# Performance work log

Hardware: AMD Instinct MI355X
Metric: run time of the kernel (lower is better)

Reference implementation:

```python
import jax, jax.numpy as jnp
import numpy as np

N, T, E = 50000, 12, 800000
IN_C, HID, OUT_C = 32, 64, 32


def setup_inputs() -> dict:
    key = jax.random.key(0)
    ks = jax.random.split(key, 20)
    def lin(k, fan_in, shape):
        b = 1.0 / np.sqrt(fan_in)
        return jax.random.uniform(k, shape, jnp.float32, -b, b)
    inp = {
        "x": jax.random.normal(ks[0], (T, N, IN_C), jnp.float32),
        "edge_index": jax.random.randint(ks[1], (T, 2, E), 0, N, jnp.int32),
        "edge_weight": jax.random.uniform(ks[2], (T, E), jnp.float32),
        # GCNConv weights (x @ W, glorot) + biases for z, r, h gates
        "Wz": lin(ks[3], IN_C, (IN_C, HID)), "bz": jnp.zeros((HID,), jnp.float32),
        "Wr": lin(ks[4], IN_C, (IN_C, HID)), "br": jnp.zeros((HID,), jnp.float32),
        "Wh": lin(ks[5], IN_C, (IN_C, HID)), "bh": jnp.zeros((HID,), jnp.float32),
        # Linear(2*hidden -> hidden) for each gate
        "Lz_w": lin(ks[6], 2 * HID, (2 * HID, HID)), "Lz_b": lin(ks[7], 2 * HID, (HID,)),
        "Lr_w": lin(ks[8], 2 * HID, (2 * HID, HID)), "Lr_b": lin(ks[9], 2 * HID, (HID,)),
        "Lh_w": lin(ks[10], 2 * HID, (2 * HID, HID)), "Lh_b": lin(ks[11], 2 * HID, (HID,)),
        # final Linear(hidden -> out)
        "W_out": lin(ks[12], HID, (HID, OUT_C)), "b_out": lin(ks[13], HID, (OUT_C,)),
    }
    return inp


def _gcn_conv(x, src, dst, ew, W, b):
    # GCNConv with add_self_loops=True, symmetric gcn_norm
    loop = jnp.arange(N, dtype=src.dtype)
    s = jnp.concatenate([src, loop])
    d = jnp.concatenate([dst, loop])
    w = jnp.concatenate([ew, jnp.ones((N,), ew.dtype)])
    deg = jax.ops.segment_sum(w, d, num_segments=N)          # [N]
    dinv = jnp.where(deg > 0, jax.lax.rsqrt(deg), 0.0)
    norm = dinv[s] * w * dinv[d]                              # [E+N]
    h = x @ W                                                 # [N, HID]
    out = jax.ops.segment_sum(h[s] * norm[:, None], d, num_segments=N)
    return out + b


def _tgcn_step(x, src, dst, ew, p):
    # H is zeros every call (model never threads hidden state)
    H = jnp.zeros((N, HID), x.dtype)
    cz = _gcn_conv(x, src, dst, ew, p["Wz"], p["bz"])
    Z = jax.nn.sigmoid(jnp.concatenate([cz, H], axis=1) @ p["Lz_w"] + p["Lz_b"])
    cr = _gcn_conv(x, src, dst, ew, p["Wr"], p["br"])
    R = jax.nn.sigmoid(jnp.concatenate([cr, H], axis=1) @ p["Lr_w"] + p["Lr_b"])
    ch = _gcn_conv(x, src, dst, ew, p["Wh"], p["bh"])
    Ht = jnp.tanh(jnp.concatenate([ch, H * R], axis=1) @ p["Lh_w"] + p["Lh_b"])
    return Z * H + (1.0 - Z) * Ht


def reference(x, edge_index, edge_weight, Wz, bz, Wr, br, Wh, bh,
              Lz_w, Lz_b, Lr_w, Lr_b, Lh_w, Lh_b, W_out, b_out):
    p = dict(Wz=Wz, bz=bz, Wr=Wr, br=br, Wh=Wh, bh=bh,
             Lz_w=Lz_w, Lz_b=Lz_b, Lr_w=Lr_w, Lr_b=Lr_b, Lh_w=Lh_w, Lh_b=Lh_b)

    def step(acc, ts):
        xt, ei, ew = ts
        out = _tgcn_step(xt, ei[0], ei[1], ew, p)
        return acc + out, None

    acc, _ = jax.lax.scan(step, jnp.zeros((N, HID), x.dtype),
                          (x, edge_index, edge_weight))
    mean = acc / T
    return mean @ W_out + b_out
```

## Files before the change

### kernel.cpp

```cpp
#include <hip/hip_runtime.h>
#include <hip/hip_fp16.h>

#define NN 50000
#define TT 12
#define EE 800000
#define IN_C 32
#define HID 64
#define OUT_C 32
#define BSZ 64
#define NB ((NN + BSZ - 1) / BSZ)
#define EPB 8192
#define ABLK ((EE + EPB - 1) / EPB)
#define BST 512
#define GT 4
#define XPAIRS ((size_t)TT * NN * 16)

typedef _Float16 half8_t __attribute__((ext_vector_type(8)));
typedef float f32x4_t __attribute__((ext_vector_type(4)));

__global__ __launch_bounds__(64) void prep_kernel(
    const float* __restrict__ Wz, const float* __restrict__ bz,
    const float* __restrict__ Lzw, const float* __restrict__ Lzb,
    const float* __restrict__ Wh, const float* __restrict__ bh,
    const float* __restrict__ Lhw, const float* __restrict__ Lhb,
    float* __restrict__ Mz, float* __restrict__ Bz,
    float* __restrict__ Mh, float* __restrict__ Bh) {
  const int j = threadIdx.x;
  const int i = blockIdx.x;
  const int h = blockIdx.y;
  const float* W  = h ? Wh  : Wz;
  const float* b  = h ? bh  : bz;
  const float* L  = h ? Lhw : Lzw;
  const float* Lb = h ? Lhb : Lzb;
  float* M = h ? Mh : Mz;
  float* B = h ? Bh : Bz;
  if (i < IN_C) {
    float v = 0.f;
    for (int k = 0; k < HID; ++k) v += W[i * HID + k] * L[k * HID + j];
    M[i * HID + j] = v;
  } else {
    float v = Lb[j];
    for (int k = 0; k < HID; ++k) v += b[k] * L[k * HID + j];
    B[j] = v;
  }
}

__global__ __launch_bounds__(64) void prep_b16_kernel(
    const float* __restrict__ Mz, const float* __restrict__ Mh,
    _Float16* __restrict__ B16) {
  int l = threadIdx.x;
  int cc = blockIdx.x;
  int g = blockIdx.y;
  const float* M = g ? Mh : Mz;
#pragma unroll
  for (int i = 0; i < 8; ++i) {
    int k = (l >> 4) * 8 + i;
    int col = cc * 16 + (l & 15);
    B16[(((size_t)g * 4 + cc) * 64 + l) * 8 + i] = (_Float16)M[k * HID + col];
  }
}

__global__ __launch_bounds__(256) void xconv_kernel(const float* __restrict__ x,
                                                    __half2* __restrict__ xh) {
  size_t i = (size_t)blockIdx.x * 256 + threadIdx.x;
  if (i < XPAIRS) {
    float2 f = ((const float2*)x)[i];
    xh[i] = __floats2half2_rn(f.x, f.y);
  }
}

__global__ __launch_bounds__(BST) void bsort_kernel(
    const int* __restrict__ ei, const float* __restrict__ ew,
    unsigned long long* __restrict__ bin2G, int* __restrict__ runoffG,
    int tbase) {
  __shared__ int hist[NB];
  __shared__ int rnk[NB];
  __shared__ int lbase[NB + 1];
  __shared__ unsigned long long sent[EPB];
  int tl = blockIdx.y;
  const int* src = ei + (size_t)(tbase + tl) * 2 * EE;
  const int* dst = src + EE;
  const float* w = ew + (size_t)(tbase + tl) * EE;
  int t = threadIdx.x;
  for (int i = t; i < NB; i += BST) { hist[i] = 0; rnk[i] = 0; }
  __syncthreads();
  int e0 = blockIdx.x * EPB;
  int cnt = min(EPB, EE - e0);
  for (int i = t; i < cnt; i += BST) atomicAdd(&hist[dst[e0 + i] >> 6], 1);
  __syncthreads();
  if (t == 0) {
    int run = 0;
    for (int b = 0; b < NB; ++b) { lbase[b] = run; run += hist[b]; }
    lbase[NB] = run;
  }
  __syncthreads();
  int* rof = runoffG + ((size_t)tl * ABLK + blockIdx.x) * (NB + 1);
  for (int b = t; b < NB + 1; b += BST) rof[b] = lbase[b];
  for (int i = t; i < cnt; i += BST) {
    int d = dst[e0 + i], s = src[e0 + i];
    int b = d >> 6;
    unsigned short hw = __half_as_ushort(__float2half_rn(w[e0 + i]));
    int pos = lbase[b] + atomicAdd(&rnk[b], 1);
    sent[pos] = (unsigned long long)((unsigned)s | ((unsigned)(d & 63) << 16)) |
                ((unsigned long long)hw << 32);
  }
  __syncthreads();
  unsigned long long* reg = bin2G + ((size_t)tl * ABLK + blockIdx.x) * EPB;
  for (int i = t; i < cnt; i += BST) reg[i] = sent[i];
}

__global__ __launch_bounds__(256) void deg_kernel(
    const int* __restrict__ runoffG, const unsigned long long* __restrict__ bin2G,
    float* __restrict__ dinvA, int* __restrict__ loffA) {
  __shared__ float wsum[BSZ];
  __shared__ int cnt[BSZ];
  __shared__ int loff[BSZ];
  int tl = blockIdx.y, b = blockIdx.x;
  int t = threadIdx.x;
  if (t < BSZ) { wsum[t] = 0.f; cnt[t] = 0; }
  __syncthreads();
  const int* runoff = runoffG + (size_t)tl * ABLK * (NB + 1);
  int g = t >> 5;
  int lane = t & 31;
  for (int blk = g; blk < ABLK; blk += 8) {
    int r0 = runoff[blk * (NB + 1) + b];
    int r1 = runoff[blk * (NB + 1) + b + 1];
    const unsigned long long* reg = bin2G + ((size_t)tl * ABLK + blk) * EPB;
    for (int i = r0 + lane; i < r1; i += 32) {
      unsigned long long u = reg[i];
      int dl = (int)((u >> 16) & 63u);
      atomicAdd(&wsum[dl], __half2float(__ushort_as_half((unsigned short)(u >> 32))));
      atomicAdd(&cnt[dl], 1);
    }
  }
  __syncthreads();
  if (t == 0) {
    int run = 0;
#pragma unroll
    for (int i = 0; i < BSZ; ++i) { loff[i] = run; run += cnt[i]; }
  }
  __syncthreads();
  int n = b * BSZ + t;
  if (t < BSZ && n < NN) {
    dinvA[(size_t)tl * NN + n] = rsqrtf(1.0f + wsum[t]);
    loffA[(size_t)tl * NN + n] = loff[t];
  }
}

__global__ __launch_bounds__(1024) void bscan_kernel(const int* __restrict__ runoffG,
                                                     int* __restrict__ bbaseA) {
  __shared__ int s[1024];
  int tl = blockIdx.x, t = threadIdx.x;
  const int* runoff = runoffG + (size_t)tl * ABLK * (NB + 1);
  int v = 0;
  if (t < NB) {
    for (int blk = 0; blk < ABLK; ++blk)
      v += runoff[blk * (NB + 1) + t + 1] - runoff[blk * (NB + 1) + t];
  }
  s[t] = v;
  __syncthreads();
  for (int o = 1; o < 1024; o <<= 1) {
    int u = (t >= o) ? s[t - o] : 0;
    __syncthreads();
    s[t] += u;
    __syncthreads();
  }
  if (t < NB) bbaseA[(size_t)tl * NB + t] = s[t] - v;
}

__global__ __launch_bounds__(256) void sort_kernel(
    const int* __restrict__ runoffG, const unsigned long long* __restrict__ bin2G,
    const float* __restrict__ dinvA, const int* __restrict__ bbaseA,
    const int* __restrict__ loffA, unsigned* __restrict__ sbufG,
    int* __restrict__ noffG) {
  __shared__ int plc[BSZ];
  int tl = blockIdx.y, b = blockIdx.x;
  int t = threadIdx.x;
  int base = bbaseA[(size_t)tl * NB + b];
  int* noff = noffG + (size_t)tl * (NN + 1);
  if (t < BSZ) {
    int n = b * BSZ + t;
    int v = (n < NN) ? base + loffA[(size_t)tl * NN + n] : base;
    plc[t] = v;
    if (n < NN) noff[n] = v;
  }
  if (b == 0 && t == 0) noff[NN] = EE;
  __syncthreads();
  const int* runoff = runoffG + (size_t)tl * ABLK * (NB + 1);
  const float* dinv = dinvA + (size_t)tl * NN;
  unsigned* sbuf = sbufG + (size_t)tl * EE;
  int g = t >> 5;
  int lane = t & 31;
  for (int blk = g; blk < ABLK; blk += 8) {
    int r0 = runoff[blk * (NB + 1) + b];
    int r1 = runoff[blk * (NB + 1) + b + 1];
    const unsigned long long* reg = bin2G + ((size_t)tl * ABLK + blk) * EPB;
    for (int i = r0 + lane; i < r1; i += 32) {
      unsigned long long u = reg[i];
      int s = (int)(u & 0xFFFFu);
      int dl = (int)((u >> 16) & 63u);
      float nm = __half2float(__ushort_as_half((unsigned short)(u >> 32))) * dinv[s];
      int pos = atomicAdd(&plc[dl], 1);
      sbuf[pos] = (unsigned)s |
                  ((unsigned)__half_as_ushort(__float2half_rn(nm)) << 16);
    }
  }
}

__global__ __launch_bounds__(256) void gather_y_kernel(
    const __half2* __restrict__ xh,
    const float* __restrict__ dinvA, const int* __restrict__ noffG,
    const unsigned* __restrict__ sbufG, __half2* __restrict__ yG, int tbase) {
  int t = threadIdx.x;
  int w = t >> 6;
  int lane = t & 63;
  int h2 = lane >> 5;
  int g = (lane >> 2) & 7;
  int cq = lane & 3;
  int tl = blockIdx.y;
  int n = blockIdx.x * 8 + w * 2 + h2;

  const float* dinv = dinvA + (size_t)tl * NN;
  const int* noff = noffG + (size_t)tl * (NN + 1);
  const unsigned* sbuf = sbufG + (size_t)tl * EE;
  const __half2* xht = xh + (size_t)(tbase + tl) * NN * 16;

  int e0 = noff[n], e1 = noff[n + 1];
  float v0 = 0.f, v1 = 0.f, v2 = 0.f, v3 = 0.f;
  float v4 = 0.f, v5 = 0.f, v6 = 0.f, v7 = 0.f;
  for (int e = e0 + g; e < e1; e += 8) {
    unsigned u = sbuf[e];
    float nm = __half2float(__ushort_as_half((unsigned short)(u >> 16)));
    uint4 xr = ((const uint4*)(xht + (size_t)(u & 0xFFFFu) * 16))[cq];
    const __half2* hp = (const __half2*)&xr;
    float2 f0 = __half22float2(hp[0]);
    float2 f1 = __half22float2(hp[1]);
    float2 f2 = __half22float2(hp[2]);
    float2 f3 = __half22float2(hp[3]);
    v0 += nm * f0.x; v1 += nm * f0.y;
    v2 += nm * f1.x; v3 += nm * f1.y;
    v4 += nm * f2.x; v5 += nm * f2.y;
    v6 += nm * f3.x; v7 += nm * f3.y;
  }
#pragma unroll
  for (int m = 4; m <= 16; m <<= 1) {
    v0 += __shfl_xor(v0, m); v1 += __shfl_xor(v1, m);
    v2 += __shfl_xor(v2, m); v3 += __shfl_xor(v3, m);
    v4 += __shfl_xor(v4, m); v5 += __shfl_xor(v5, m);
    v6 += __shfl_xor(v6, m); v7 += __shfl_xor(v7, m);
  }
  if (g == 0) {
    float dv = dinv[n];
    uint4 xs = ((const uint4*)(xht + (size_t)n * 16))[cq];
    const __half2* hs = (const __half2*)&xs;
    float2 s0 = __half22float2(hs[0]);
    float2 s1 = __half22float2(hs[1]);
    float2 s2 = __half22float2(hs[2]);
    float2 s3 = __half22float2(hs[3]);
    __half2 o[4];
    o[0] = __floats2half2_rn(dv * (v0 + dv * s0.x), dv * (v1 + dv * s0.y));
    o[1] = __floats2half2_rn(dv * (v2 + dv * s1.x), dv * (v3 + dv * s1.y));
    o[2] = __floats2half2_rn(dv * (v4 + dv * s2.x), dv * (v5 + dv * s2.y));
    o[3] = __floats2half2_rn(dv * (v6 + dv * s3.x), dv * (v7 + dv * s3.y));
    __half2* yp = yG + ((size_t)tl * NN + n) * 16 + cq * 4;
    *(uint4*)yp = *(const uint4*)o;
  }
}

__global__ __launch_bounds__(256) void gate_acc_kernel(
    const __half2* __restrict__ yG, const _Float16* __restrict__ B16,
    const float* __restrict__ Bz, const float* __restrict__ Bh,
    float* __restrict__ acc, int c) {
  int t = threadIdx.x;
  int w = t >> 6;
  int lane = t & 63;
  int nb = blockIdx.x * BSZ;
  int t0 = blockIdx.y * GT;
  int te = min(t0 + GT, c);

  half8_t bf[8];
#pragma unroll
  for (int q = 0; q < 8; ++q)
    bf[q] = *(const half8_t*)(B16 + ((size_t)q * 64 + lane) * 8);
  float bzv[4], bhv[4];
#pragma unroll
  for (int cc = 0; cc < 4; ++cc) {
    bzv[cc] = Bz[cc * 16 + (lane & 15)];
    bhv[cc] = Bh[cc * 16 + (lane & 15)];
  }
  float accr[16];
#pragma unroll
  for (int k = 0; k < 16; ++k) accr[k] = 0.f;

  const _Float16* yF = (const _Float16*)yG;
  int arow = nb + w * 16 + (lane & 15);
  if (arow >= NN) arow = NN - 1;
  int koff = (lane >> 4) * 8;

  for (int tl = t0; tl < te; ++tl) {
    half8_t a = *(const half8_t*)(yF + ((size_t)tl * NN + arow) * 32 + koff);
    f32x4_t dz0 = {0.f, 0.f, 0.f, 0.f};
    f32x4_t dz[4], dh[4];
#pragma unroll
    for (int cc = 0; cc < 4; ++cc) {
      dz[cc] = __builtin_amdgcn_mfma_f32_16x16x32_f16(a, bf[cc], dz0, 0, 0, 0);
      dh[cc] = __builtin_amdgcn_mfma_f32_16x16x32_f16(a, bf[4 + cc], dz0, 0, 0, 0);
    }
#pragma unroll
    for (int cc = 0; cc < 4; ++cc) {
#pragma unroll
      for (int r = 0; r < 4; ++r) {
        float za = dz[cc][r] + bzv[cc];
        float ha = dh[cc][r] + bhv[cc];
        float z = 1.0f / (1.0f + __expf(-za));
        float th = 1.0f - 2.0f / (__expf(2.f * ha) + 1.0f);
        accr[cc * 4 + r] += (1.0f - z) * th;
      }
    }
  }
#pragma unroll
  for (int cc = 0; cc < 4; ++cc) {
#pragma unroll
    for (int r = 0; r < 4; ++r) {
      int n = nb + w * 16 + (lane >> 4) * 4 + r;
      int j = cc * 16 + (lane & 15);
      if (n < NN) atomicAdd(&acc[(size_t)n * HID + j], accr[cc * 4 + r]);
    }
  }
}

__global__ __launch_bounds__(256) void out_kernel(const float* __restrict__ acc,
                                                  const float* __restrict__ W_out,
                                                  const float* __restrict__ b_out,
                                                  float* __restrict__ out) {
  __shared__ float sW[HID * OUT_C], sB[OUT_C];
  for (int i = threadIdx.x; i < HID * OUT_C; i += 256) sW[i] = W_out[i];
  if (threadIdx.x < OUT_C) sB[threadIdx.x] = b_out[threadIdx.x];
  __syncthreads();
  unsigned tid = blockIdx.x * 256u + threadIdx.x;
  unsigned n = tid >> 5;
  int o = tid & 31;
  if (n >= NN) return;
  const float* ar = acc + (size_t)n * HID;
  float v = 0.f;
#pragma unroll
  for (int k = 0; k < HID; ++k) v += ar[k] * sW[k * OUT_C + o];
  out[(size_t)n * OUT_C + o] = v * (1.0f / (float)TT) + sB[o];
}

static inline char* alignp(char* p, size_t a) {
  return (char*)(((size_t)p + a - 1) & ~(a - 1));
}

extern "C" void kernel_launch(void* const* d_in, const int* in_sizes, int n_in,
                              void* d_out, int out_size, void* d_ws, size_t ws_size,
                              hipStream_t stream) {
  const float* x     = (const float*)d_in[0];
  const int*   ei    = (const int*)d_in[1];
  const float* ew    = (const float*)d_in[2];
  const float* Wz    = (const float*)d_in[3];
  const float* bz    = (const float*)d_in[4];
  const float* Wh    = (const float*)d_in[7];
  const float* bh    = (const float*)d_in[8];
  const float* Lz_w  = (const float*)d_in[9];
  const float* Lz_b  = (const float*)d_in[10];
  const float* Lh_w  = (const float*)d_in[13];
  const float* Lh_b  = (const float*)d_in[14];
  const float* W_out = (const float*)d_in[15];
  const float* b_out = (const float*)d_in[16];
  float* out = (float*)d_out;

  const size_t noffB  = (size_t)(NN + 1) * 4;
  const size_t dinvB  = (size_t)NN * 4;
  const size_t loffB  = (size_t)NN * 4;
  const size_t bbB    = (size_t)NB * 4;
  const size_t rofB   = (size_t)ABLK * (NB + 1) * 4;
  const size_t sbufB  = (size_t)EE * 4;
  const size_t bin2B  = (size_t)ABLK * EPB * 8;
  const size_t perT   = noffB + dinvB + loffB + bbB + rofB + sbufB + bin2B;
  const size_t xhB    = XPAIRS * 4;
  const size_t fixedB = 4 * ((size_t)2 * IN_C * HID + 2 * HID)
                      + 8192 + (size_t)NN * HID * 4 + xhB + 4096;

  int nt = 12;
  if (ws_size < fixedB + 12 * perT) {
    nt = (int)((ws_size - fixedB) / perT);
    if (nt < 1) nt = 1;
    if (nt > 12) nt = 12;
  }

  char* p = (char*)d_ws;
  unsigned long long* bin2 = (unsigned long long*)p;
  p += bin2B * nt;
  int* noffG  = (int*)p;          p += noffB * nt;
  float* dinv = (float*)p;        p += dinvB * nt;
  int* loffG  = (int*)p;          p += loffB * nt;
  int* bbase  = (int*)p;          p += bbB * nt;
  int* runoff = (int*)p;          p += rofB * nt;
  unsigned* sbufG = (unsigned*)p; p += sbufB * nt;
  p = alignp(p, 16);
  _Float16* B16 = (_Float16*)p;   p += 8192;
  float* Mz = (float*)p;
  float* Mh = Mz + IN_C * HID;
  float* Bz = Mh + IN_C * HID;
  float* Bh = Bz + HID;
  float* acc = Bh + HID;
  p = alignp((char*)(acc + (size_t)NN * HID), 256);
  __half2* xh = (__half2*)p;
  __half2* yG = (__half2*)bin2;

  prep_kernel<<<dim3(IN_C + 1, 2), 64, 0, stream>>>(Wz, bz, Lz_w, Lz_b, Wh, bh,
                                                    Lh_w, Lh_b, Mz, Bz, Mh, Bh);
  prep_b16_kernel<<<dim3(4, 2), 64, 0, stream>>>(Mz, Mh, B16);
  xconv_kernel<<<(unsigned)((XPAIRS + 255) / 256), 256, 0, stream>>>(x, xh);
  hipMemsetAsync(acc, 0, (size_t)NN * HID * sizeof(float), stream);

  for (int tb = 0; tb < TT; tb += nt) {
    int c = (TT - tb < nt) ? (TT - tb) : nt;
    bsort_kernel<<<dim3(ABLK, c), BST, 0, stream>>>(ei, ew, bin2, runoff, tb);
    deg_kernel<<<dim3(NB, c), 256, 0, stream>>>(runoff, bin2, dinv, loffG);
    bscan_kernel<<<c, 1024, 0, stream>>>(runoff, bbase);
    sort_kernel<<<dim3(NB, c), 256, 0, stream>>>(runoff, bin2, dinv, bbase,
                                                 loffG, sbufG, noffG);
    gather_y_kernel<<<dim3(NN / 8, c), 256, 0, stream>>>(xh, dinv, noffG,
                                                         sbufG, yG, tb);
    gate_acc_kernel<<<dim3(NB, (c + GT - 1) / GT), 256, 0, stream>>>(
        yG, B16, Bz, Bh, acc, c);
  }

  out_kernel<<<(NN * OUT_C + 255) / 256, 256, 0, stream>>>(acc, W_out, b_out, out);
}
```

Before: 533.4 us.

## Fuse degree and sort kernels, defer source-dinv scaling to gather

Merges deg_kernel and sort_kernel into one sortdeg_kernel that computes per-node weight sums and local offsets in shared memory, then scatters edges in the same block. The loffA buffer and one launch go away, and the binned edge list is read twice inside one block instead of across two kernels. Because dinv[src] is not yet known during sorting, the source-side dinv multiply moves into gather_y_kernel, which adds a random dinv load per edge there. The sort now stores the raw half edge weight.

```diff
diff --git a/kernel.cpp b/kernel.cpp
--- a/kernel.cpp
+++ b/kernel.cpp
@@ -109,11 +109,34 @@
   for (int i = t; i < cnt; i += BST) reg[i] = sent[i];
 }
 
-__global__ __launch_bounds__(256) void deg_kernel(
+__global__ __launch_bounds__(1024) void bscan_kernel(const int* __restrict__ runoffG,
+                                                     int* __restrict__ bbaseA) {
+  __shared__ int s[1024];
+  int tl = blockIdx.x, t = threadIdx.x;
+  const int* runoff = runoffG + (size_t)tl * ABLK * (NB + 1);
+  int v = 0;
+  if (t < NB) {
+    for (int blk = 0; blk < ABLK; ++blk)
+      v += runoff[blk * (NB + 1) + t + 1] - runoff[blk * (NB + 1) + t];
+  }
+  s[t] = v;
+  __syncthreads();
+  for (int o = 1; o < 1024; o <<= 1) {
+    int u = (t >= o) ? s[t - o] : 0;
+    __syncthreads();
+    s[t] += u;
+    __syncthreads();
+  }
+  if (t < NB) bbaseA[(size_t)tl * NB + t] = s[t] - v;
+}
+
+__global__ __launch_bounds__(256) void sortdeg_kernel(
     const int* __restrict__ runoffG, const unsigned long long* __restrict__ bin2G,
-    float* __restrict__ dinvA, int* __restrict__ loffA) {
+    const int* __restrict__ bbaseA, float* __restrict__ dinvA,
+    unsigned* __restrict__ sbufG, int* __restrict__ noffG) {
   __shared__ float wsum[BSZ];
   __shared__ int cnt[BSZ];
+  __shared__ int plc[BSZ];
   __shared__ int loff[BSZ];
   int tl = blockIdx.y, b = blockIdx.x;
   int t = threadIdx.x;
@@ -140,69 +163,28 @@
     for (int i = 0; i < BSZ; ++i) { loff[i] = run; run += cnt[i]; }
   }
   __syncthreads();
-  int n = b * BSZ + t;
-  if (t < BSZ && n < NN) {
-    dinvA[(size_t)tl * NN + n] = rsqrtf(1.0f + wsum[t]);
-    loffA[(size_t)tl * NN + n] = loff[t];
-  }
-}
-
-__global__ __launch_bounds__(1024) void bscan_kernel(const int* __restrict__ runoffG,
-                                                     int* __restrict__ bbaseA) {
-  __shared__ int s[1024];
-  int tl = blockIdx.x, t = threadIdx.x;
-  const int* runoff = runoffG + (size_t)tl * ABLK * (NB + 1);
-  int v = 0;
-  if (t < NB) {
-    for (int blk = 0; blk < ABLK; ++blk)
-      v += runoff[blk * (NB + 1) + t + 1] - runoff[blk * (NB + 1) + t];
-  }
-  s[t] = v;
-  __syncthreads();
-  for (int o = 1; o < 1024; o <<= 1) {
-    int u = (t >= o) ? s[t - o] : 0;
-    __syncthreads();
-    s[t] += u;
-    __syncthreads();
-  }
-  if (t < NB) bbaseA[(size_t)tl * NB + t] = s[t] - v;
-}
-
-__global__ __launch_bounds__(256) void sort_kernel(
-    const int* __restrict__ runoffG, const unsigned long long* __restrict__ bin2G,
-    const float* __restrict__ dinvA, const int* __restrict__ bbaseA,
-    const int* __restrict__ loffA, unsigned* __restrict__ sbufG,
-    int* __restrict__ noffG) {
-  __shared__ int plc[BSZ];
-  int tl = blockIdx.y, b = blockIdx.x;
-  int t = threadIdx.x;
   int base = bbaseA[(size_t)tl * NB + b];
   int* noff = noffG + (size_t)tl * (NN + 1);
   if (t < BSZ) {
     int n = b * BSZ + t;
-    int v = (n < NN) ? base + loffA[(size_t)tl * NN + n] : base;
+    int v = base + loff[t];
     plc[t] = v;
-    if (n < NN) noff[n] = v;
+    if (n < NN) {
+      noff[n] = v;
+      dinvA[(size_t)tl * NN + n] = rsqrtf(1.0f + wsum[t]);
+    }
   }
   if (b == 0 && t == 0) noff[NN] = EE;
   __syncthreads();
-  const int* runoff = runoffG + (size_t)tl * ABLK * (NB + 1);
-  const float* dinv = dinvA + (size_t)tl * NN;
   unsigned* sbuf = sbufG + (size_t)tl * EE;
-  int g = t >> 5;
-  int lane = t & 31;
   for (int blk = g; blk < ABLK; blk += 8) {
     int r0 = runoff[blk * (NB + 1) + b];
     int r1 = runoff[blk * (NB + 1) + b + 1];
     const unsigned long long* reg = bin2G + ((size_t)tl * ABLK + blk) * EPB;
     for (int i = r0 + lane; i < r1; i += 32) {
       unsigned long long u = reg[i];
-      int s = (int)(u & 0xFFFFu);
-      int dl = (int)((u >> 16) & 63u);
-      float nm = __half2float(__ushort_as_half((unsigned short)(u >> 32))) * dinv[s];
-      int pos = atomicAdd(&plc[dl], 1);
-      sbuf[pos] = (unsigned)s |
-                  ((unsigned)__half_as_ushort(__float2half_rn(nm)) << 16);
+      int pos = atomicAdd(&plc[(int)((u >> 16) & 63u)], 1);
+      sbuf[pos] = (unsigned)(u & 0xFFFFu) | ((unsigned)(u >> 32) << 16);
     }
   }
 }
@@ -230,8 +212,9 @@
   float v4 = 0.f, v5 = 0.f, v6 = 0.f, v7 = 0.f;
   for (int e = e0 + g; e < e1; e += 8) {
     unsigned u = sbuf[e];
-    float nm = __half2float(__ushort_as_half((unsigned short)(u >> 16)));
-    uint4 xr = ((const uint4*)(xht + (size_t)(u & 0xFFFFu) * 16))[cq];
+    int s = (int)(u & 0xFFFFu);
+    float nm = __half2float(__ushort_as_half((unsigned short)(u >> 16))) * dinv[s];
+    uint4 xr = ((const uint4*)(xht + (size_t)s * 16))[cq];
     const __half2* hp = (const __half2*)&xr;
     float2 f0 = __half22float2(hp[0]);
     float2 f1 = __half22float2(hp[1]);
@@ -372,12 +355,11 @@
 
   const size_t noffB  = (size_t)(NN + 1) * 4;
   const size_t dinvB  = (size_t)NN * 4;
-  const size_t loffB  = (size_t)NN * 4;
   const size_t bbB    = (size_t)NB * 4;
   const size_t rofB   = (size_t)ABLK * (NB + 1) * 4;
   const size_t sbufB  = (size_t)EE * 4;
   const size_t bin2B  = (size_t)ABLK * EPB * 8;
-  const size_t perT   = noffB + dinvB + loffB + bbB + rofB + sbufB + bin2B;
+  const size_t perT   = noffB + dinvB + bbB + rofB + sbufB + bin2B;
   const size_t xhB    = XPAIRS * 4;
   const size_t fixedB = 4 * ((size_t)2 * IN_C * HID + 2 * HID)
                       + 8192 + (size_t)NN * HID * 4 + xhB + 4096;
@@ -394,7 +376,6 @@
   p += bin2B * nt;
   int* noffG  = (int*)p;          p += noffB * nt;
   float* dinv = (float*)p;        p += dinvB * nt;
-  int* loffG  = (int*)p;          p += loffB * nt;
   int* bbase  = (int*)p;          p += bbB * nt;
   int* runoff = (int*)p;          p += rofB * nt;
   unsigned* sbufG = (unsigned*)p; p += sbufB * nt;
@@ -418,10 +399,9 @@
   for (int tb = 0; tb < TT; tb += nt) {
     int c = (TT - tb < nt) ? (TT - tb) : nt;
     bsort_kernel<<<dim3(ABLK, c), BST, 0, stream>>>(ei, ew, bin2, runoff, tb);
-    deg_kernel<<<dim3(NB, c), 256, 0, stream>>>(runoff, bin2, dinv, loffG);
     bscan_kernel<<<c, 1024, 0, stream>>>(runoff, bbase);
-    sort_kernel<<<dim3(NB, c), 256, 0, stream>>>(runoff, bin2, dinv, bbase,
-                                                 loffG, sbufG, noffG);
+    sortdeg_kernel<<<dim3(NB, c), 256, 0, stream>>>(runoff, bin2, bbase,
+                                                    dinv, sbufG, noffG);
     gather_y_kernel<<<dim3(NN / 8, c), 256, 0, stream>>>(xh, dinv, noffG,
                                                          sbufG, yG, tb);
     gate_acc_kernel<<<dim3(NB, (c + GT - 1) / GT), 256, 0, stream>>>(
```

After: 492.6 us, median of 2. -7.7%, faster.
